# Kernel optimization log

Hardware: AMD Instinct MI355X
Metric: run time of the kernel (lower is better)

Reference implementation:

```python
import jax, jax.numpy as jnp
import numpy as np

HEAD_SIZE = 128


def _rope(t, cos, sin):
    # t: [B, T, D]; cos/sin: [T, D//2]; rotate interleaved (even, odd) pairs
    t2 = t.reshape(t.shape[0], t.shape[1], -1, 2)
    x0, x1 = t2[..., 0], t2[..., 1]
    c = cos[None, :, :]
    s = sin[None, :, :]
    out = jnp.stack([x0 * c - x1 * s, x0 * s + x1 * c], axis=-1)
    return out.reshape(t.shape)


def setup_inputs() -> dict:
    key = jax.random.key(0)
    ks = jax.random.split(key, 4)
    B, T, E, D = 4, 4096, 1024, HEAD_SIZE
    x = jax.random.normal(ks[0], (B, T, E), dtype=jnp.float32)
    Wq = jax.random.normal(ks[1], (E, D), dtype=jnp.float32) * (E ** -0.5)
    Wk = jax.random.normal(ks[2], (E, D), dtype=jnp.float32) * (E ** -0.5)
    Wv = jax.random.normal(ks[3], (E, D), dtype=jnp.float32) * (E ** -0.5)
    # RoPE frequencies as in llama-style precompute_freqs_cis
    inv_freq = 1.0 / (10000.0 ** (np.arange(0, D, 2, dtype=np.float32) / D))
    angles = np.outer(np.arange(T, dtype=np.float32), inv_freq)  # [T, D//2]
    freqs_cos = jnp.asarray(np.cos(angles), dtype=jnp.float32)
    freqs_sin = jnp.asarray(np.sin(angles), dtype=jnp.float32)
    return {"x": x, "Wq": Wq, "Wk": Wk, "Wv": Wv,
            "freqs_cos": freqs_cos, "freqs_sin": freqs_sin}


def reference(x, Wq, Wk, Wv, freqs_cos, freqs_sin):
    T = x.shape[1]
    q = x @ Wq  # [B,T,D]
    k = x @ Wk
    v = x @ Wv
    q = _rope(q, freqs_cos, freqs_sin)
    k = _rope(k, freqs_cos, freqs_sin)
    scores = jnp.einsum('bqd,bkd->bqk', q, k) * (HEAD_SIZE ** -0.5)
    causal = jnp.tril(jnp.ones((T, T), dtype=bool))  # [T,T]
    scores = jnp.where(causal[None, :, :], scores, -jnp.inf)
    probs = jax.nn.softmax(scores, axis=-1)  # dropout p=0 -> identity
    return jnp.einsum('bqk,bkd->bqd', probs, v)
```

## Files before the change

kernel.cpp:

```cpp
#include <hip/hip_runtime.h>
#include <hip/hip_bf16.h>

#define T_SEQ   4096
#define B_BATCH 4
#define E_DIM   1024
#define D_HEAD  128
#define BT      (B_BATCH * T_SEQ)
#define CHUNK   512
#define KVB     32

using bf16x8 = __attribute__((ext_vector_type(8))) short;
using f32x4  = __attribute__((ext_vector_type(4))) float;

static __device__ __forceinline__ unsigned short f2bf(float f) {
    unsigned int b = __float_as_uint(f);
    return (unsigned short)((b + 0x7FFFu + ((b >> 16) & 1u)) >> 16);
}
static __device__ __forceinline__ float bf2f(unsigned short u) {
    return __uint_as_float(((unsigned int)u) << 16);
}
static __device__ __forceinline__ void split2(float f, unsigned short &h, unsigned short &l) {
    unsigned int b = __float_as_uint(f);
    h = (unsigned short)(b >> 16);
    l = f2bf(f - __uint_as_float(b & 0xFFFF0000u));
}
static __device__ __forceinline__ void split8(const float4 &a, const float4 &b,
                                              uint4 &hi, uint4 &lo) {
    float fa[8] = {a.x, a.y, a.z, a.w, b.x, b.y, b.z, b.w};
    unsigned int h[4], l[4];
    #pragma unroll
    for (int i = 0; i < 4; ++i) {
        unsigned short h0, h1, l0, l1;
        split2(fa[2 * i],     h0, l0);
        split2(fa[2 * i + 1], h1, l1);
        h[i] = (unsigned int)h0 | ((unsigned int)h1 << 16);
        l[i] = (unsigned int)l0 | ((unsigned int)l1 << 16);
    }
    hi = make_uint4(h[0], h[1], h[2], h[3]);
    lo = make_uint4(l[0], l[1], l[2], l[3]);
}

__global__ __launch_bounds__(256) void prep_w_kernel(
    const float* __restrict__ Wq, const float* __restrict__ Wk,
    const float* __restrict__ Wv,
    unsigned short* __restrict__ wth, unsigned short* __restrict__ wtl)
{
    const int zi = blockIdx.z;
    const float* __restrict__ W = (zi == 0) ? Wq : (zi == 1) ? Wk : Wv;
    const int k0 = blockIdx.x * 64;
    const int n0 = blockIdx.y * 32;
    const int t  = threadIdx.x;
    __shared__ float S[64][36];

    #pragma unroll
    for (int i = 0; i < 2; ++i) {
        int f = t + i * 256;
        int r = f >> 3, c4 = f & 7;
        *(float4*)&S[r][c4 * 4] = *(const float4*)&W[(size_t)(k0 + r) * D_HEAD + n0 + c4 * 4];
    }
    __syncthreads();

    int n = t >> 3, kc = t & 7;
    unsigned int h[4], l[4];
    #pragma unroll
    for (int i = 0; i < 4; ++i) {
        unsigned short h0, h1, l0, l1;
        split2(S[kc * 8 + 2 * i][n],     h0, l0);
        split2(S[kc * 8 + 2 * i + 1][n], h1, l1);
        h[i] = (unsigned int)h0 | ((unsigned int)h1 << 16);
        l[i] = (unsigned int)l0 | ((unsigned int)l1 << 16);
    }
    size_t ofs = ((size_t)zi * 128 + n0 + n) * 1024 + k0 + kc * 8;
    *(uint4*)&wth[ofs] = make_uint4(h[0], h[1], h[2], h[3]);
    *(uint4*)&wtl[ofs] = make_uint4(l[0], l[1], l[2], l[3]);
}

__global__ __launch_bounds__(256) void qkv_gemm_kernel(
    const float* __restrict__ x,
    const unsigned short* __restrict__ wth, const unsigned short* __restrict__ wtl,
    const float* __restrict__ fcos, const float* __restrict__ fsin,
    unsigned short* __restrict__ qh, unsigned short* __restrict__ qlo,
    unsigned short* __restrict__ kh, unsigned short* __restrict__ klo,
    unsigned short* __restrict__ vb)
{
    const int zi   = blockIdx.y;
    const int row0 = blockIdx.x * 64;
    const unsigned short* __restrict__ Bhg = wth + (size_t)zi * 128 * 1024;
    const unsigned short* __restrict__ Blg = wtl + (size_t)zi * 128 * 1024;

    __shared__ unsigned short Ah[64 * 32], Al[64 * 32];
    __shared__ unsigned short Bh[128 * 32], Bl[128 * 32];

    const int tid  = threadIdx.x;
    const int lane = tid & 63;
    const int w    = tid >> 6;
    const int wr   = w >> 1, wc = w & 1;
    const int colq = lane & 15;
    const int g    = lane >> 4;

    f32x4 acc[2][4];
    #pragma unroll
    for (int m = 0; m < 2; ++m)
        #pragma unroll
        for (int n = 0; n < 4; ++n) acc[m][n] = (f32x4){0.f, 0.f, 0.f, 0.f};

    const int ra = tid >> 2, ca = tid & 3;
    const int sa = ca ^ ((ra >> 1) & 3);
    char* AhB = (char*)Ah; char* AlB = (char*)Al;
    char* BhB = (char*)Bh; char* BlB = (char*)Bl;

    for (int k0 = 0; k0 < E_DIM; k0 += 32) {
        {
            const float* xp = &x[(size_t)(row0 + ra) * E_DIM + k0 + ca * 8];
            float4 a0 = *(const float4*)xp;
            float4 a1 = *(const float4*)(xp + 4);
            uint4 hi, lo;
            split8(a0, a1, hi, lo);
            *(uint4*)(AhB + ra * 64 + sa * 16) = hi;
            *(uint4*)(AlB + ra * 64 + sa * 16) = lo;
        }
        #pragma unroll
        for (int i = 0; i < 2; ++i) {
            int j  = tid + i * 256;
            int rb = j >> 2, cb = j & 3;
            int sb = cb ^ ((rb >> 1) & 3);
            size_t gofs = (size_t)rb * 1024 + k0 + cb * 8;
            *(uint4*)(BhB + rb * 64 + sb * 16) = *(const uint4*)&Bhg[gofs];
            *(uint4*)(BlB + rb * 64 + sb * 16) = *(const uint4*)&Blg[gofs];
        }
        __syncthreads();

        bf16x8 afh[2], afl[2], bfh[4], bfl[4];
        #pragma unroll
        for (int m = 0; m < 2; ++m) {
            int rowA = wr * 32 + m * 16 + colq;
            int off  = rowA * 64 + (g ^ ((rowA >> 1) & 3)) * 16;
            afh[m] = *(const bf16x8*)(AhB + off);
            afl[m] = *(const bf16x8*)(AlB + off);
        }
        #pragma unroll
        for (int n = 0; n < 4; ++n) {
            int rowB = wc * 64 + n * 16 + colq;
            int off  = rowB * 64 + (g ^ ((rowB >> 1) & 3)) * 16;
            bfh[n] = *(const bf16x8*)(BhB + off);
            bfl[n] = *(const bf16x8*)(BlB + off);
        }
        #pragma unroll
        for (int m = 0; m < 2; ++m)
            #pragma unroll
            for (int n = 0; n < 4; ++n) {
                acc[m][n] = __builtin_amdgcn_mfma_f32_16x16x32_bf16(afh[m], bfh[n], acc[m][n], 0, 0, 0);
                acc[m][n] = __builtin_amdgcn_mfma_f32_16x16x32_bf16(afl[m], bfh[n], acc[m][n], 0, 0, 0);
                acc[m][n] = __builtin_amdgcn_mfma_f32_16x16x32_bf16(afh[m], bfl[n], acc[m][n], 0, 0, 0);
            }
        __syncthreads();
    }

    const float SCALE = 0.08838834764831845f;
    #pragma unroll
    for (int m = 0; m < 2; ++m)
        #pragma unroll
        for (int n = 0; n < 4; ++n) {
            int col = wc * 64 + n * 16 + colq;
            int h   = col >> 1;
            #pragma unroll
            for (int r = 0; r < 4; ++r) {
                int row = row0 + wr * 32 + m * 16 + g * 4 + r;
                int t   = row & (T_SEQ - 1);
                float val = acc[m][n][r];
                size_t ofs = (size_t)row * D_HEAD + col;
                if (zi == 2) {
                    vb[ofs] = f2bf(val);
                } else {
                    float partner = __shfl_xor(val, 1, 64);
                    float c = fcos[t * 64 + h];
                    float s = fsin[t * 64 + h];
                    float o = (col & 1) ? (partner * s + val * c)
                                        : (val * c - partner * s);
                    if (zi == 0) o *= SCALE;
                    unsigned short hv, lv;
                    split2(o, hv, lv);
                    if (zi == 0) { qh[ofs] = hv; qlo[ofs] = lv; }
                    else         { kh[ofs] = hv; klo[ofs] = lv; }
                }
            }
        }
}

__global__ __launch_bounds__(256) void vtrans_kernel(
    const unsigned short* __restrict__ vb,
    unsigned short* __restrict__ vt)
{
    const int t0 = (blockIdx.x & 63) * 64;
    const int b  = blockIdx.x >> 6;
    const int tid = threadIdx.x;
    __shared__ unsigned short S[64][132];

    #pragma unroll
    for (int i = 0; i < 8; ++i) {
        int idx = tid + i * 256;
        int t  = idx >> 5;
        int c4 = idx & 31;
        *reinterpret_cast<ushort4*>(&S[t][c4 * 4]) =
            *reinterpret_cast<const ushort4*>(&vb[(size_t)(b * T_SEQ + t0 + t) * 128 + c4 * 4]);
    }
    __syncthreads();
    #pragma unroll
    for (int i = 0; i < 8; ++i) {
        int idx = tid + i * 256;
        int d = idx >> 4;
        int c = idx & 15;
        ushort4 val;
        val.x = S[c * 4 + 0][d];
        val.y = S[c * 4 + 1][d];
        val.z = S[c * 4 + 2][d];
        val.w = S[c * 4 + 3][d];
        *reinterpret_cast<ushort4*>(&vt[((size_t)(b * 128 + d)) * T_SEQ + t0 + c * 4]) = val;
    }
}

__global__ __launch_bounds__(128, 2) void attn_chunk_kernel(
    const unsigned short* __restrict__ qh, const unsigned short* __restrict__ qlo,
    const unsigned short* __restrict__ kh, const unsigned short* __restrict__ klo,
    const unsigned short* __restrict__ vt,
    float* __restrict__ opart,
    float* __restrict__ mlpart)
{
    const int bid = blockIdx.x;
    const int c   = bid & 7;
    const int qt  = (bid >> 3) & 63;
    const int b   = bid >> 9;
    const int kstart = c * CHUNK;
    const int qend   = qt * 64 + 64;
    if (kstart >= qend) return;
    const int kend   = min(kstart + CHUNK, qend);
    const int ntiles = (kend - kstart) >> 5;

    const int tid  = threadIdx.x;
    const int w    = tid >> 6;
    const int lane = tid & 63;
    const int col  = lane & 15;
    const int g    = lane >> 4;
    const int qbw  = qt * 64 + w * 32;

    __shared__ unsigned short Kh[KVB * 128];
    __shared__ unsigned short Kl[KVB * 128];
    __shared__ unsigned short Vts[128 * 40];
    __shared__ unsigned short Pl[2][1024];

    bf16x8 qhf[2][4], qlf[2][4];
    #pragma unroll
    for (int s = 0; s < 2; ++s) {
        size_t qrow = (size_t)(b * T_SEQ + qbw + s * 16 + col);
        #pragma unroll
        for (int dc = 0; dc < 4; ++dc) {
            int off = dc * 32 + g * 8;
            qhf[s][dc] = *reinterpret_cast<const bf16x8*>(&qh [qrow * 128 + off]);
            qlf[s][dc] = *reinterpret_cast<const bf16x8*>(&qlo[qrow * 128 + off]);
        }
    }

    f32x4 oacc[2][8];
    #pragma unroll
    for (int s = 0; s < 2; ++s)
        #pragma unroll
        for (int db = 0; db < 8; ++db)
            oacc[s][db] = (f32x4){0.f, 0.f, 0.f, 0.f};
    float m_s[2] = {-3.0e38f, -3.0e38f};
    float l_s[2] = {0.f, 0.f};

    char* KhB  = reinterpret_cast<char*>(Kh);
    char* KlB  = reinterpret_cast<char*>(Kl);
    char* VtB  = reinterpret_cast<char*>(Vts);
    char* PlB  = reinterpret_cast<char*>(Pl[w]);

    for (int t = 0; t < ntiles; ++t) {
        const int kbase = kstart + t * KVB;

        #pragma unroll
        for (int i = 0; i < 4; ++i) {
            int idx = tid + i * 128;
            int key = idx >> 4, c16 = idx & 15;
            size_t gofs = ((size_t)(b * T_SEQ + kbase + key)) * 128 + c16 * 8;
            int lofs = (key * 256 + c16 * 16) ^ ((key & 7) << 4);
            *reinterpret_cast<uint4*>(KhB + lofs) = *reinterpret_cast<const uint4*>(&kh [gofs]);
            *reinterpret_cast<uint4*>(KlB + lofs) = *reinterpret_cast<const uint4*>(&klo[gofs]);
        }
        #pragma unroll
        for (int i = 0; i < 4; ++i) {
            int idx = tid + i * 128;
            int d = idx >> 2, c16 = idx & 3;
            size_t gofs = ((size_t)(b * 128 + d)) * T_SEQ + kbase + c16 * 8;
            int lofs = d * 80 + c16 * 16;
            *reinterpret_cast<uint4*>(VtB + lofs) = *reinterpret_cast<const uint4*>(&vt[gofs]);
        }
        __syncthreads();

        f32x4 st[2][2];
        st[0][0] = (f32x4){0,0,0,0}; st[0][1] = (f32x4){0,0,0,0};
        st[1][0] = (f32x4){0,0,0,0}; st[1][1] = (f32x4){0,0,0,0};
        #pragma unroll
        for (int kb = 0; kb < 2; ++kb) {
            #pragma unroll
            for (int dc = 0; dc < 4; ++dc) {
                int lofs = ((kb * 16 + col) * 256 + dc * 64 + g * 16) ^ ((col & 7) << 4);
                bf16x8 khf = *reinterpret_cast<const bf16x8*>(KhB + lofs);
                bf16x8 klf = *reinterpret_cast<const bf16x8*>(KlB + lofs);
                #pragma unroll
                for (int s = 0; s < 2; ++s) {
                    st[s][kb] = __builtin_amdgcn_mfma_f32_16x16x32_bf16(khf, qhf[s][dc], st[s][kb], 0, 0, 0);
                    st[s][kb] = __builtin_amdgcn_mfma_f32_16x16x32_bf16(klf, qhf[s][dc], st[s][kb], 0, 0, 0);
                    st[s][kb] = __builtin_amdgcn_mfma_f32_16x16x32_bf16(khf, qlf[s][dc], st[s][kb], 0, 0, 0);
                }
            }
        }

        #pragma unroll
        for (int s = 0; s < 2; ++s) {
            int qg = qbw + s * 16 + col;
            #pragma unroll
            for (int kb = 0; kb < 2; ++kb) {
                int keyb = kbase + kb * 16 + g * 4;
                #pragma unroll
                for (int r = 0; r < 4; ++r)
                    if (keyb + r > qg) st[s][kb][r] = -3.0e38f;
            }
            float tmax = st[s][0][0];
            #pragma unroll
            for (int kb = 0; kb < 2; ++kb)
                #pragma unroll
                for (int r = 0; r < 4; ++r) tmax = fmaxf(tmax, st[s][kb][r]);
            tmax = fmaxf(tmax, __shfl_xor(tmax, 16, 64));
            tmax = fmaxf(tmax, __shfl_xor(tmax, 32, 64));
            float mnew = fmaxf(m_s[s], tmax);
            float corr = __expf(m_s[s] - mnew);
            m_s[s] = mnew;
            float psum = 0.f;
            #pragma unroll
            for (int kb = 0; kb < 2; ++kb)
                #pragma unroll
                for (int r = 0; r < 4; ++r) {
                    float e = __expf(st[s][kb][r] - mnew);
                    st[s][kb][r] = e;
                    psum += e;
                }
            psum += __shfl_xor(psum, 16, 64);
            psum += __shfl_xor(psum, 32, 64);
            l_s[s] = l_s[s] * corr + psum;

            #pragma unroll
            for (int r = 0; r < 4; ++r) {
                float cr = __shfl(corr, (lane & 48) + g * 4 + r, 64);
                #pragma unroll
                for (int db = 0; db < 8; ++db) oacc[s][db][r] *= cr;
            }

            int q = s * 16 + col;
            #pragma unroll
            for (int kb = 0; kb < 2; ++kb) {
                unsigned int pk0 = (unsigned int)f2bf(st[s][kb][0]) | ((unsigned int)f2bf(st[s][kb][1]) << 16);
                unsigned int pk1 = (unsigned int)f2bf(st[s][kb][2]) | ((unsigned int)f2bf(st[s][kb][3]) << 16);
                int base = q * 64 + (kb * 16 + g * 4) * 2;
                int sw = (q & 3) << 4;
                *reinterpret_cast<unsigned int*>(PlB + ((base    ) ^ sw)) = pk0;
                *reinterpret_cast<unsigned int*>(PlB + ((base + 4) ^ sw)) = pk1;
            }
        }

        #pragma unroll
        for (int db = 0; db < 8; ++db) {
            int d = db * 16 + col;
            bf16x8 vf = *reinterpret_cast<const bf16x8*>(VtB + d * 80 + g * 16);
            #pragma unroll
            for (int s = 0; s < 2; ++s) {
                int lofs = ((s * 16 + col) * 64 + g * 16) ^ ((col & 3) << 4);
                bf16x8 pf = *reinterpret_cast<const bf16x8*>(PlB + lofs);
                oacc[s][db] = __builtin_amdgcn_mfma_f32_16x16x32_bf16(pf, vf, oacc[s][db], 0, 0, 0);
            }
        }
        __syncthreads();
    }

    const int pb = (b * 64 + qt) * 8 + c;
    float* op = opart + (size_t)pb * (64 * 128);
    #pragma unroll
    for (int s = 0; s < 2; ++s)
        #pragma unroll
        for (int db = 0; db < 8; ++db)
            #pragma unroll
            for (int r = 0; r < 4; ++r) {
                int qloc = w * 32 + s * 16 + g * 4 + r;
                op[qloc * 128 + db * 16 + col] = oacc[s][db][r];
            }
    if (g == 0) {
        float* ml = mlpart + (size_t)pb * 128;
        #pragma unroll
        for (int s = 0; s < 2; ++s) {
            ml[     w * 32 + s * 16 + col] = m_s[s];
            ml[64 + w * 32 + s * 16 + col] = l_s[s];
        }
    }
}

__global__ __launch_bounds__(256) void combine_kernel(
    const float* __restrict__ opart, const float* __restrict__ mlpart,
    float* __restrict__ out)
{
    const int qt  = blockIdx.x & 63;
    const int b   = blockIdx.x >> 6;
    const int nch = (qt >> 3) + 1;
    const int tid = threadIdx.x;
    const int q   = tid >> 2;
    const int d0  = (tid & 3) * 32;
    const int pb0 = (b * 64 + qt) * 8;

    float mv[8], wv[8];
    float M = -3.0e38f;
    #pragma unroll
    for (int cc = 0; cc < 8; ++cc)
        if (cc < nch) {
            mv[cc] = mlpart[(size_t)(pb0 + cc) * 128 + q];
            M = fmaxf(M, mv[cc]);
        }
    float L = 0.f;
    #pragma unroll
    for (int cc = 0; cc < 8; ++cc)
        if (cc < nch) {
            float wgt = __expf(mv[cc] - M);
            wv[cc] = wgt;
            L += mlpart[(size_t)(pb0 + cc) * 128 + 64 + q] * wgt;
        }
    float invL = 1.f / L;

    float4 acc[8];
    #pragma unroll
    for (int i = 0; i < 8; ++i) acc[i] = make_float4(0.f, 0.f, 0.f, 0.f);
    #pragma unroll
    for (int cc = 0; cc < 8; ++cc)
        if (cc < nch) {
            const float4* src = reinterpret_cast<const float4*>(
                &opart[((size_t)(pb0 + cc) * 64 + q) * 128 + d0]);
            float wgt = wv[cc] * invL;
            #pragma unroll
            for (int i = 0; i < 8; ++i) {
                float4 v = src[i];
                acc[i].x += wgt * v.x; acc[i].y += wgt * v.y;
                acc[i].z += wgt * v.z; acc[i].w += wgt * v.w;
            }
        }
    float4* dst = reinterpret_cast<float4*>(&out[((size_t)(b * T_SEQ + qt * 64 + q)) * 128 + d0]);
    #pragma unroll
    for (int i = 0; i < 8; ++i) dst[i] = acc[i];
}

extern "C" void kernel_launch(void* const* d_in, const int* in_sizes, int n_in,
                              void* d_out, int out_size, void* d_ws, size_t ws_size,
                              hipStream_t stream)
{
    (void)in_sizes; (void)n_in; (void)out_size; (void)ws_size;
    const float* x  = (const float*)d_in[0];
    const float* Wq = (const float*)d_in[1];
    const float* Wk = (const float*)d_in[2];
    const float* Wv = (const float*)d_in[3];
    const float* fc = (const float*)d_in[4];
    const float* fs = (const float*)d_in[5];
    float* out = (float*)d_out;

    const size_t NW = (size_t)3 * 128 * 1024;
    const size_t NE = (size_t)BT * 128;
    unsigned short* wth = (unsigned short*)d_ws;
    unsigned short* wtl = wth + NW;
    unsigned short* qh  = wtl + NW;
    unsigned short* qlo = qh  + NE;
    unsigned short* kh  = qlo + NE;
    unsigned short* klo = kh  + NE;
    unsigned short* vb  = klo + NE;
    unsigned short* vt  = vb  + NE;
    float* opart  = (float*)(vt + NE);
    float* mlpart = opart + (size_t)2048 * 64 * 128;

    prep_w_kernel<<<dim3(16, 4, 3), 256, 0, stream>>>(Wq, Wk, Wv, wth, wtl);
    qkv_gemm_kernel<<<dim3(BT / 64, 3), 256, 0, stream>>>(
        x, wth, wtl, fc, fs, qh, qlo, kh, klo, vb);
    vtrans_kernel<<<256, 256, 0, stream>>>(vb, vt);
    attn_chunk_kernel<<<2048, 128, 0, stream>>>(qh, qlo, kh, klo, vt, opart, mlpart);
    combine_kernel<<<256, 256, 0, stream>>>(opart, mlpart, out);
}
```

Measured before the change: 324.1 us.

## Widen attention blocks to 128 queries, prefetch K/V tiles, lazy rescale

```diff
diff --git a/kernel.cpp b/kernel.cpp
--- a/kernel.cpp
+++ b/kernel.cpp
@@ -219,7 +219,7 @@
     }
 }
 
-__global__ __launch_bounds__(128, 2) void attn_chunk_kernel(
+__global__ __launch_bounds__(256) void attn_chunk_kernel(
     const unsigned short* __restrict__ qh, const unsigned short* __restrict__ qlo,
     const unsigned short* __restrict__ kh, const unsigned short* __restrict__ klo,
     const unsigned short* __restrict__ vt,
@@ -228,10 +228,10 @@
 {
     const int bid = blockIdx.x;
     const int c   = bid & 7;
-    const int qt  = (bid >> 3) & 63;
-    const int b   = bid >> 9;
+    const int qt  = (bid >> 3) & 31;
+    const int b   = bid >> 8;
     const int kstart = c * CHUNK;
-    const int qend   = qt * 64 + 64;
+    const int qend   = qt * 128 + 128;
     if (kstart >= qend) return;
     const int kend   = min(kstart + CHUNK, qend);
     const int ntiles = (kend - kstart) >> 5;
@@ -241,12 +241,38 @@
     const int lane = tid & 63;
     const int col  = lane & 15;
     const int g    = lane >> 4;
-    const int qbw  = qt * 64 + w * 32;
+    const int qbw  = qt * 128 + w * 32;
 
     __shared__ unsigned short Kh[KVB * 128];
     __shared__ unsigned short Kl[KVB * 128];
     __shared__ unsigned short Vts[128 * 40];
-    __shared__ unsigned short Pl[2][1024];
+    __shared__ unsigned short Pl[4][1024];
+
+    char* KhB = reinterpret_cast<char*>(Kh);
+    char* KlB = reinterpret_cast<char*>(Kl);
+    char* VtB = reinterpret_cast<char*>(Vts);
+    char* PlB = reinterpret_cast<char*>(Pl[w]);
+
+    int kkey[2], kc16[2], klofs[2], vd[2], vcc[2], vlofs[2];
+    #pragma unroll
+    for (int i = 0; i < 2; ++i) {
+        int j = tid + i * 256;
+        kkey[i]  = j >> 4;  kc16[i] = j & 15;
+        klofs[i] = (kkey[i] * 256 + kc16[i] * 16) ^ ((kkey[i] & 7) << 4);
+        vd[i]    = j >> 2;  vcc[i]  = j & 3;
+        vlofs[i] = vd[i] * 80 + vcc[i] * 16;
+    }
+    uint4 pkh[2], pkl[2], pv[2];
+    auto fetch = [&](int kbase) {
+        #pragma unroll
+        for (int i = 0; i < 2; ++i) {
+            size_t gk = ((size_t)(b * T_SEQ + kbase + kkey[i])) * 128 + kc16[i] * 8;
+            pkh[i] = *reinterpret_cast<const uint4*>(&kh [gk]);
+            pkl[i] = *reinterpret_cast<const uint4*>(&klo[gk]);
+            size_t gv = ((size_t)(b * 128 + vd[i])) * T_SEQ + kbase + vcc[i] * 8;
+            pv[i]  = *reinterpret_cast<const uint4*>(&vt[gv]);
+        }
+    };
 
     bf16x8 qhf[2][4], qlf[2][4];
     #pragma unroll
@@ -269,32 +295,20 @@
     float m_s[2] = {-3.0e38f, -3.0e38f};
     float l_s[2] = {0.f, 0.f};
 
-    char* KhB  = reinterpret_cast<char*>(Kh);
-    char* KlB  = reinterpret_cast<char*>(Kl);
-    char* VtB  = reinterpret_cast<char*>(Vts);
-    char* PlB  = reinterpret_cast<char*>(Pl[w]);
+    fetch(kstart);
 
     for (int t = 0; t < ntiles; ++t) {
         const int kbase = kstart + t * KVB;
 
-        #pragma unroll
-        for (int i = 0; i < 4; ++i) {
-            int idx = tid + i * 128;
-            int key = idx >> 4, c16 = idx & 15;
-            size_t gofs = ((size_t)(b * T_SEQ + kbase + key)) * 128 + c16 * 8;
-            int lofs = (key * 256 + c16 * 16) ^ ((key & 7) << 4);
-            *reinterpret_cast<uint4*>(KhB + lofs) = *reinterpret_cast<const uint4*>(&kh [gofs]);
-            *reinterpret_cast<uint4*>(KlB + lofs) = *reinterpret_cast<const uint4*>(&klo[gofs]);
-        }
-        #pragma unroll
-        for (int i = 0; i < 4; ++i) {
-            int idx = tid + i * 128;
-            int d = idx >> 2, c16 = idx & 3;
-            size_t gofs = ((size_t)(b * 128 + d)) * T_SEQ + kbase + c16 * 8;
-            int lofs = d * 80 + c16 * 16;
-            *reinterpret_cast<uint4*>(VtB + lofs) = *reinterpret_cast<const uint4*>(&vt[gofs]);
-        }
         __syncthreads();
+        #pragma unroll
+        for (int i = 0; i < 2; ++i) {
+            *reinterpret_cast<uint4*>(KhB + klofs[i]) = pkh[i];
+            *reinterpret_cast<uint4*>(KlB + klofs[i]) = pkl[i];
+            *reinterpret_cast<uint4*>(VtB + vlofs[i]) = pv[i];
+        }
+        __syncthreads();
+        if (t + 1 < ntiles) fetch(kbase + KVB);
 
         f32x4 st[2][2];
         st[0][0] = (f32x4){0,0,0,0}; st[0][1] = (f32x4){0,0,0,0};
@@ -317,13 +331,17 @@
 
         #pragma unroll
         for (int s = 0; s < 2; ++s) {
-            int qg = qbw + s * 16 + col;
-            #pragma unroll
-            for (int kb = 0; kb < 2; ++kb) {
-                int keyb = kbase + kb * 16 + g * 4;
+            const int qg = qbw + s * 16 + col;
+            if (kbase + KVB - 1 > qbw + s * 16) {
                 #pragma unroll
-                for (int r = 0; r < 4; ++r)
-                    if (keyb + r > qg) st[s][kb][r] = -3.0e38f;
+                for (int kb = 0; kb < 2; ++kb) {
+                    if (kbase + kb * 16 + 15 > qbw + s * 16) {
+                        int keyb = kbase + kb * 16 + g * 4;
+                        #pragma unroll
+                        for (int r = 0; r < 4; ++r)
+                            if (keyb + r > qg) st[s][kb][r] = -3.0e38f;
+                    }
+                }
             }
             float tmax = st[s][0][0];
             #pragma unroll
@@ -332,28 +350,31 @@
                 for (int r = 0; r < 4; ++r) tmax = fmaxf(tmax, st[s][kb][r]);
             tmax = fmaxf(tmax, __shfl_xor(tmax, 16, 64));
             tmax = fmaxf(tmax, __shfl_xor(tmax, 32, 64));
-            float mnew = fmaxf(m_s[s], tmax);
-            float corr = __expf(m_s[s] - mnew);
-            m_s[s] = mnew;
+
+            if (!__all(tmax <= m_s[s] + 8.0f)) {
+                float mnew = fmaxf(m_s[s], tmax);
+                float corr = __expf(m_s[s] - mnew);
+                m_s[s] = mnew;
+                l_s[s] *= corr;
+                #pragma unroll
+                for (int r = 0; r < 4; ++r) {
+                    float cr = __shfl(corr, (lane & 48) + g * 4 + r, 64);
+                    #pragma unroll
+                    for (int db = 0; db < 8; ++db) oacc[s][db][r] *= cr;
+                }
+            }
             float psum = 0.f;
             #pragma unroll
             for (int kb = 0; kb < 2; ++kb)
                 #pragma unroll
                 for (int r = 0; r < 4; ++r) {
-                    float e = __expf(st[s][kb][r] - mnew);
+                    float e = __expf(st[s][kb][r] - m_s[s]);
                     st[s][kb][r] = e;
                     psum += e;
                 }
             psum += __shfl_xor(psum, 16, 64);
             psum += __shfl_xor(psum, 32, 64);
-            l_s[s] = l_s[s] * corr + psum;
-
-            #pragma unroll
-            for (int r = 0; r < 4; ++r) {
-                float cr = __shfl(corr, (lane & 48) + g * 4 + r, 64);
-                #pragma unroll
-                for (int db = 0; db < 8; ++db) oacc[s][db][r] *= cr;
-            }
+            l_s[s] += psum;
 
             int q = s * 16 + col;
             #pragma unroll
@@ -378,11 +399,10 @@
                 oacc[s][db] = __builtin_amdgcn_mfma_f32_16x16x32_bf16(pf, vf, oacc[s][db], 0, 0, 0);
             }
         }
-        __syncthreads();
-    }
-
-    const int pb = (b * 64 + qt) * 8 + c;
-    float* op = opart + (size_t)pb * (64 * 128);
+    }
+
+    const int pb = (b * 32 + qt) * 8 + c;
+    float* op = opart + (size_t)pb * (128 * 128);
     #pragma unroll
     for (int s = 0; s < 2; ++s)
         #pragma unroll
@@ -393,11 +413,11 @@
                 op[qloc * 128 + db * 16 + col] = oacc[s][db][r];
             }
     if (g == 0) {
-        float* ml = mlpart + (size_t)pb * 128;
+        float* ml = mlpart + (size_t)pb * 256;
         #pragma unroll
         for (int s = 0; s < 2; ++s) {
-            ml[     w * 32 + s * 16 + col] = m_s[s];
-            ml[64 + w * 32 + s * 16 + col] = l_s[s];
+            ml[      w * 32 + s * 16 + col] = m_s[s];
+            ml[128 + w * 32 + s * 16 + col] = l_s[s];
         }
     }
 }
@@ -406,20 +426,20 @@
     const float* __restrict__ opart, const float* __restrict__ mlpart,
     float* __restrict__ out)
 {
-    const int qt  = blockIdx.x & 63;
-    const int b   = blockIdx.x >> 6;
-    const int nch = (qt >> 3) + 1;
+    const int qt  = blockIdx.x & 31;
+    const int b   = blockIdx.x >> 5;
+    const int nch = ((qt * 128 + 127) >> 9) + 1;
     const int tid = threadIdx.x;
-    const int q   = tid >> 2;
-    const int d0  = (tid & 3) * 32;
-    const int pb0 = (b * 64 + qt) * 8;
+    const int q   = tid >> 1;
+    const int d0  = (tid & 1) * 64;
+    const int pb0 = (b * 32 + qt) * 8;
 
     float mv[8], wv[8];
     float M = -3.0e38f;
     #pragma unroll
     for (int cc = 0; cc < 8; ++cc)
         if (cc < nch) {
-            mv[cc] = mlpart[(size_t)(pb0 + cc) * 128 + q];
+            mv[cc] = mlpart[(size_t)(pb0 + cc) * 256 + q];
             M = fmaxf(M, mv[cc]);
         }
     float L = 0.f;
@@ -428,29 +448,29 @@
         if (cc < nch) {
             float wgt = __expf(mv[cc] - M);
             wv[cc] = wgt;
-            L += mlpart[(size_t)(pb0 + cc) * 128 + 64 + q] * wgt;
+            L += mlpart[(size_t)(pb0 + cc) * 256 + 128 + q] * wgt;
         }
     float invL = 1.f / L;
 
-    float4 acc[8];
-    #pragma unroll
-    for (int i = 0; i < 8; ++i) acc[i] = make_float4(0.f, 0.f, 0.f, 0.f);
+    float4 acc[16];
+    #pragma unroll
+    for (int i = 0; i < 16; ++i) acc[i] = make_float4(0.f, 0.f, 0.f, 0.f);
     #pragma unroll
     for (int cc = 0; cc < 8; ++cc)
         if (cc < nch) {
             const float4* src = reinterpret_cast<const float4*>(
-                &opart[((size_t)(pb0 + cc) * 64 + q) * 128 + d0]);
+                &opart[((size_t)(pb0 + cc) * 128 + q) * 128 + d0]);
             float wgt = wv[cc] * invL;
             #pragma unroll
-            for (int i = 0; i < 8; ++i) {
+            for (int i = 0; i < 16; ++i) {
                 float4 v = src[i];
                 acc[i].x += wgt * v.x; acc[i].y += wgt * v.y;
                 acc[i].z += wgt * v.z; acc[i].w += wgt * v.w;
             }
         }
-    float4* dst = reinterpret_cast<float4*>(&out[((size_t)(b * T_SEQ + qt * 64 + q)) * 128 + d0]);
-    #pragma unroll
-    for (int i = 0; i < 8; ++i) dst[i] = acc[i];
+    float4* dst = reinterpret_cast<float4*>(&out[((size_t)(b * T_SEQ + qt * 128 + q)) * 128 + d0]);
+    #pragma unroll
+    for (int i = 0; i < 16; ++i) dst[i] = acc[i];
 }
 
 extern "C" void kernel_launch(void* const* d_in, const int* in_sizes, int n_in,
@@ -477,12 +497,12 @@
     unsigned short* vb  = klo + NE;
     unsigned short* vt  = vb  + NE;
     float* opart  = (float*)(vt + NE);
-    float* mlpart = opart + (size_t)2048 * 64 * 128;
+    float* mlpart = opart + (size_t)1024 * 128 * 128;
 
     prep_w_kernel<<<dim3(16, 4, 3), 256, 0, stream>>>(Wq, Wk, Wv, wth, wtl);
     qkv_gemm_kernel<<<dim3(BT / 64, 3), 256, 0, stream>>>(
         x, wth, wtl, fc, fs, qh, qlo, kh, klo, vb);
     vtrans_kernel<<<256, 256, 0, stream>>>(vb, vt);
-    attn_chunk_kernel<<<2048, 128, 0, stream>>>(qh, qlo, kh, klo, vt, opart, mlpart);
-    combine_kernel<<<256, 256, 0, stream>>>(opart, mlpart, out);
-}
+    attn_chunk_kernel<<<1024, 256, 0, stream>>>(qh, qlo, kh, klo, vt, opart, mlpart);
+    combine_kernel<<<128, 256, 0, stream>>>(opart, mlpart, out);
+}
```

Measured after the change: 411.7 us. +27.0%, slower.
